# Optimization experiments

Measured on AMD Instinct MI355X. Metric: run time of the kernel, lower is better.

## Reference

```python
import jax, jax.numpy as jnp
import numpy as np

N = 3072      # nodes
F = 256       # nfeat
H = 8         # heads
H1 = 128      # hidden layer 1 (per head)
H2 = 128      # hidden layer 2 (per head)
OUT = 64      # out_att output dim
ALPHA = 0.2   # LeakyReLU slope
NEG = -9e15   # mask fill (as in dense GAT)


def setup_inputs() -> dict:
    key = jax.random.key(0)
    ks = jax.random.split(key, 11)
    x = jax.random.normal(ks[0], (N, F), jnp.float32)
    adj = jax.random.bernoulli(ks[1], 0.05, (N, N)).astype(jnp.float32)
    observation = jax.random.randint(ks[2], (1, N), 0, 2).astype(jnp.int32)
    s_mat = jax.random.bernoulli(ks[3], 0.05, (N, N)).astype(jnp.float32)  # unused (method='base')
    theta = jax.random.uniform(ks[4], (1, F), jnp.float32)
    W0 = jax.random.normal(ks[5], (H, F, H1), jnp.float32) * 0.05
    a0 = jax.random.normal(ks[6], (H, 2 * H1, 1), jnp.float32) * 0.05
    W1 = jax.random.normal(ks[7], (H, H1, H2), jnp.float32) * 0.05
    a1 = jax.random.normal(ks[8], (H, 2 * H2, 1), jnp.float32) * 0.05
    Wo = jax.random.normal(ks[9], (H * H2, OUT), jnp.float32) * 0.05
    ao = jax.random.normal(ks[10], (2 * OUT, 1), jnp.float32) * 0.05
    return {"x": x, "adj": adj, "observation": observation, "s_mat": s_mat,
            "theta": theta, "W0": W0, "a0": a0, "W1": W1, "a1": a1,
            "Wo": Wo, "ao": ao}


def _gat_layer(h, mask, W, a, concat):
    # Dense GAT layer: Wh = hW; e_ij = LeakyReLU(a1.Wh_i + a2.Wh_j); masked softmax; aggregate.
    Wh = h @ W                      # [N, d]
    d = W.shape[-1]
    f1 = Wh @ a[:d]                 # [N, 1]
    f2 = Wh @ a[d:]                 # [N, 1]
    e = jax.nn.leaky_relu(f1 + f2.T, ALPHA)           # [N, N]
    att = jax.nn.softmax(jnp.where(mask, e, NEG), axis=-1)
    hp = att @ Wh                   # [N, d]
    return jax.nn.elu(hp) if concat else hp


def reference(x, adj, observation, s_mat, theta, W0, a0, W1, a1, Wo, ao):
    mask = adj > 0
    # mergeState: add theta to rows of x in the seed set
    seed = (observation[0] == 1).astype(x.dtype)[:, None]   # [N, 1]
    h = x + seed * theta                                    # [N, F]
    # 8 heads, 2 stacked inner layers each (concat=True -> ELU inside)
    h0 = jax.vmap(lambda W, a: _gat_layer(h, mask, W, a, True))(W0, a0)          # [H, N, H1]
    h1 = jax.vmap(lambda hh, W, a: _gat_layer(hh, mask, W, a, True))(h0, W1, a1)  # [H, N, H2]
    hc = jnp.transpose(h1, (1, 0, 2)).reshape(N, H * H2)    # concat heads along features
    out = _gat_layer(hc, mask, Wo, ao, False)               # [N, OUT]
    return jax.nn.elu(out)
```

## Files before the change

### kernel.cpp

```cpp
#include <hip/hip_runtime.h>
#include <hip/hip_bf16.h>

#define NN 3072
#define NWORD 96
#define HH 8

typedef short short8 __attribute__((ext_vector_type(8)));
typedef float float4v __attribute__((ext_vector_type(4)));
typedef unsigned short ushort4v __attribute__((ext_vector_type(4)));

__device__ __forceinline__ float bf2f(unsigned short u) {
  union { unsigned u; float f; } v; v.u = ((unsigned)u) << 16; return v.f;
}
__device__ __forceinline__ unsigned short f2bf(float f) {
  union { float f; unsigned u; } v; v.f = f;
  unsigned r = v.u + 0x7fffu + ((v.u >> 16) & 1u);
  return (unsigned short)(r >> 16);
}
__device__ __forceinline__ float ldin(const void* p, size_t i, int isbf) {
  return isbf ? bf2f(((const unsigned short*)p)[i]) : ((const float*)p)[i];
}

__global__ __launch_bounds__(256) void k_detect(const unsigned* __restrict__ aw,
                                                int* __restrict__ flag) {
  __shared__ int s;
  if (threadIdx.x == 0) s = 0;
  __syncthreads();
  int any = 0;
  for (int i = threadIdx.x; i < 16384; i += 256)
    any |= ((aw[i] & 0xFFFFu) != 0u);
  if (any) s = 1;
  __syncthreads();
  if (threadIdx.x == 0) *flag = s;
}

__global__ __launch_bounds__(256) void k_mask(const void* __restrict__ adj,
                                              const int* __restrict__ flag,
                                              unsigned* __restrict__ maskT) {
  int isbf = *flag;
  int t = threadIdx.x;
  int lane = t & 63;
  for (int chunk = blockIdx.x; chunk < NN * 12; chunk += gridDim.x) {
    int row = chunk / 12;
    int seg = chunk - row * 12;
    int j = seg * 256 + t;
    bool pred = ldin(adj, (size_t)row * NN + j, isbf) != 0.f;
    unsigned long long b = __ballot(pred);
    int word = seg * 8 + (t >> 6) * 2;
    if (lane == 0) maskT[(size_t)word * NN + row] = (unsigned)b;
    else if (lane == 32) maskT[(size_t)(word + 1) * NN + row] = (unsigned)(b >> 32);
  }
}

__global__ __launch_bounds__(256) void k_prep(const void* __restrict__ x,
                                              const int* __restrict__ obs,
                                              const void* __restrict__ theta,
                                              const void* __restrict__ W0,
                                              const void* __restrict__ W1,
                                              const void* __restrict__ Wo,
                                              const int* __restrict__ flag,
                                              unsigned short* __restrict__ h_bf,
                                              unsigned short* __restrict__ W0T,
                                              unsigned short* __restrict__ W1T,
                                              unsigned short* __restrict__ WoT) {
  __shared__ __align__(16) unsigned short tile[16][17];
  int isbf = *flag;
  int t = threadIdx.x;
  int b = blockIdx.x;
  if (b < NN / 4) {
    for (int i = b * 1024 + t; i < b * 1024 + 1024; i += 256) {
      int row = i >> 8, c = i & 255;
      float v = ldin(x, i, isbf);
      if (obs[row] == 1) v += ldin(theta, c, isbf);
      h_bf[i] = f2bf(v);
    }
    return;
  }
  b -= NN / 4;
  const void* in; unsigned short* out; int R, C, r0, c0;
  if (b < 1024) {
    int h = b >> 7, rem = b & 127;
    in = (const char*)W0 + (size_t)h * 256 * 128 * (isbf ? 2 : 4);
    out = W0T + (size_t)h * 256 * 128;
    R = 256; C = 128; r0 = (rem >> 3) * 16; c0 = (rem & 7) * 16;
  } else if (b < 1536) {
    b -= 1024;
    int h = b >> 6, rem = b & 63;
    in = (const char*)W1 + (size_t)h * 128 * 128 * (isbf ? 2 : 4);
    out = W1T + (size_t)h * 128 * 128;
    R = 128; C = 128; r0 = (rem >> 3) * 16; c0 = (rem & 7) * 16;
  } else {
    b -= 1536;
    in = Wo; out = WoT;
    R = 1024; C = 64; r0 = (b >> 2) * 16; c0 = (b & 3) * 16;
  }
  int tc = t & 15, tr = t >> 4;
  tile[tr][tc] = f2bf(ldin(in, (size_t)(r0 + tr) * C + (c0 + tc), isbf));
  __syncthreads();
  out[(size_t)(c0 + tr) * R + (r0 + tc)] = tile[tc][tr];
}

template<int K>
__global__ __launch_bounds__(256) void k_gemm_fused(const unsigned short* __restrict__ A,
                                                    const unsigned short* __restrict__ WT,
                                                    unsigned short* __restrict__ WhTf,
                                                    long aOff, long wOff,
                                                    const void* __restrict__ avec,
                                                    const int* __restrict__ flag,
                                                    float* __restrict__ f1,
                                                    float* __restrict__ f2) {
  __shared__ __align__(16) unsigned short tile[4][2][32][17];
  __shared__ float avs[256];
  __shared__ float fp[2][8][32];
  int isbf = *flag;
  int head = blockIdx.x % HH;
  int jb = blockIdx.x / HH;
  A += (size_t)head * aOff; WT += (size_t)head * wOff;
  int rowbase = jb * 32;
  int t = threadIdx.x;
  int w = t >> 6, lane = t & 63;
  int q = lane >> 4, l = lane & 15;
  int colbase = w * 32;
  avs[t] = ldin(avec, (size_t)head * 256 + t, isbf);
  float4v acc[2][2];
#pragma unroll
  for (int rt = 0; rt < 2; rt++)
#pragma unroll
    for (int ct = 0; ct < 2; ct++) { float4v z = {0.f, 0.f, 0.f, 0.f}; acc[rt][ct] = z; }

  for (int kb = 0; kb < K; kb += 32) {
    short8 af[2], bfr[2];
#pragma unroll
    for (int rt = 0; rt < 2; rt++)
      af[rt] = *(const short8*)(A + (size_t)(rowbase + rt * 16 + l) * K + kb + q * 8);
#pragma unroll
    for (int ct = 0; ct < 2; ct++)
      bfr[ct] = *(const short8*)(WT + (size_t)(colbase + ct * 16 + l) * K + kb + q * 8);
#pragma unroll
    for (int rt = 0; rt < 2; rt++)
#pragma unroll
      for (int ct = 0; ct < 2; ct++)
        acc[rt][ct] = __builtin_amdgcn_mfma_f32_16x16x32_bf16(af[rt], bfr[ct], acc[rt][ct], 0, 0, 0);
  }
#pragma unroll
  for (int rt = 0; rt < 2; rt++)
#pragma unroll
    for (int ct = 0; ct < 2; ct++)
#pragma unroll
      for (int reg = 0; reg < 4; reg++)
        tile[w][ct][rt * 16 + q * 4 + reg][l] = f2bf(acc[rt][ct][reg]);
  __syncthreads();
#pragma unroll
  for (int ct = 0; ct < 2; ct++) {
    short8 r8;
#pragma unroll
    for (int i = 0; i < 8; i++) r8[i] = tile[w][ct][q * 8 + i][l];
    size_t chunk = ((size_t)head * (NN / 32) + jb) * 8 + (w * 2 + ct);
    *(short8*)(WhTf + chunk * 512 + lane * 8) = r8;
  }
  {
    int r = t & 31, g = t >> 5;
    int ww = g >> 1, cc = g & 1;
    float s1 = 0.f, s2 = 0.f;
#pragma unroll
    for (int li = 0; li < 16; li++) {
      float v = bf2f(tile[ww][cc][r][li]);
      s1 += v * avs[g * 16 + li];
      s2 += v * avs[128 + g * 16 + li];
    }
    fp[0][g][r] = s1; fp[1][g][r] = s2;
  }
  __syncthreads();
  if (t < 32) {
    float s1 = 0.f, s2 = 0.f;
#pragma unroll
    for (int g2 = 0; g2 < 8; g2++) { s1 += fp[0][g2][t]; s2 += fp[1][g2][t]; }
    f1[head * NN + rowbase + t] = s1;
    f2[head * NN + rowbase + t] = s2;
  }
}

template<int K, int KS>
__global__ __launch_bounds__(256) void k_gemm_out(const unsigned short* __restrict__ A,
                                                  const unsigned short* __restrict__ WT,
                                                  float* __restrict__ gpart) {
  constexpr int KC = K / KS;
  int ks = blockIdx.y;
  int rowbase = blockIdx.x * 16;
  int t = threadIdx.x;
  int w = t >> 6, lane = t & 63;
  int q = lane >> 4, l = lane & 15;
  int colbase = w * 16;
  float4v acc = {0.f, 0.f, 0.f, 0.f};
  for (int kb = ks * KC; kb < ks * KC + KC; kb += 32) {
    short8 af = *(const short8*)(A + (size_t)(rowbase + l) * K + kb + q * 8);
    short8 bfr = *(const short8*)(WT + (size_t)(colbase + l) * K + kb + q * 8);
    acc = __builtin_amdgcn_mfma_f32_16x16x32_bf16(af, bfr, acc, 0, 0, 0);
  }
#pragma unroll
  for (int reg = 0; reg < 4; reg++) {
    int r = rowbase + q * 4 + reg;
    int n = colbase + l;
    gpart[((size_t)ks * 64 + n) * NN + r] = acc[reg];
  }
}

template<int KS>
__global__ __launch_bounds__(256) void k_gemm_red(const float* __restrict__ gpart,
                                                  unsigned short* __restrict__ WhoTf) {
  int tid = blockIdx.x * 256 + threadIdx.x;
  int r = tid % NN, n = tid / NN;
  float s = 0.f;
#pragma unroll
  for (int ks = 0; ks < KS; ks++) s += gpart[((size_t)ks * 64 + n) * NN + r];
  int jb = r >> 5, q = (r >> 3) & 3, i = r & 7, ct = n >> 4, l = n & 15;
  WhoTf[((size_t)(jb * 4 + ct)) * 512 + (q * 16 + l) * 8 + i] = f2bf(s);
}

template<int DC>
__global__ __launch_bounds__(256) void k_f12f(const unsigned short* __restrict__ WhTf,
                                              const void* __restrict__ avec,
                                              const int* __restrict__ flag,
                                              float* __restrict__ f1, float* __restrict__ f2) {
  constexpr int NCT = DC / 16;
  int isbf = *flag;
  int head = blockIdx.y;
  int w = threadIdx.x >> 6, lane = threadIdx.x & 63;
  int q = lane >> 4, l = lane & 15;
  int jbIdx = blockIdx.x * 4 + w;
  size_t abase = (size_t)head * 2 * DC;
  float s1[8], s2[8];
#pragma unroll
  for (int i = 0; i < 8; i++) { s1[i] = 0.f; s2[i] = 0.f; }
#pragma unroll
  for (int ct = 0; ct < NCT; ct++) {
    short8 v = *(const short8*)(WhTf + (((size_t)head * (NN / 32) + jbIdx) * NCT + ct) * 512 + lane * 8);
    float a1v = ldin(avec, abase + ct * 16 + l, isbf);
    float a2v = ldin(avec, abase + DC + ct * 16 + l, isbf);
#pragma unroll
    for (int i = 0; i < 8; i++) {
      float f = bf2f((unsigned short)v[i]);
      s1[i] += f * a1v;
      s2[i] += f * a2v;
    }
  }
#pragma unroll
  for (int d = 1; d < 16; d <<= 1)
#pragma unroll
    for (int i = 0; i < 8; i++) {
      s1[i] += __shfl_xor(s1[i], d, 64);
      s2[i] += __shfl_xor(s2[i], d, 64);
    }
  if (l == 0) {
    int r = jbIdx * 32 + q * 8;
#pragma unroll
    for (int i = 0; i < 8; i++) {
      f1[head * NN + r + i] = s1[i];
      f2[head * NN + r + i] = s2[i];
    }
  }
}

template<int DCOL, int S>
__global__ __launch_bounds__(256, 4) void k_attn_part(
    const unsigned* __restrict__ maskT,
    const float* __restrict__ f1g, const float* __restrict__ f2g,
    const unsigned short* __restrict__ WhTf,
    unsigned short* __restrict__ pnum, float* __restrict__ pden, int NH) {
  constexpr int NCT = DCOL / 16;
  constexpr int JCH = NN / S;
  constexpr int NIT = JCH / 32;
  constexpr int CH = NCT * 512;
  constexpr int GR = CH / (256 * 8);
  __shared__ __align__(16) unsigned short Bs[2][CH];
  __shared__ __align__(16) float f2s[JCH];
  __shared__ unsigned ms[NIT * 64];

  int blk = blockIdx.x;
  int head = blk % NH;
  int rest = blk / NH;
  int js = rest % S;
  int bx = rest / S;
  int t = threadIdx.x;
  int w = t >> 6, lane = t & 63;
  int q = lane >> 4, l = lane & 15;
  int rowblk = bx * 64;
  int rowbase = rowblk + w * 16;
  size_t headJB = (size_t)head * (NN / 32);
  int j0 = js * JCH;

  for (int i = t; i < JCH; i += 256) f2s[i] = f2g[head * NN + j0 + i];
  for (int i = t; i < NIT * 64; i += 256)
    ms[i] = maskT[(size_t)((j0 >> 5) + (i >> 6)) * NN + rowblk + (i & 63)];
  float f1c = f1g[head * NN + rowbase + l] * 1.44269504f;

  short8 ones;
#pragma unroll
  for (int i = 0; i < 8; i++) ones[i] = (short)0x3F80;

  float4v acc[NCT];
#pragma unroll
  for (int ct = 0; ct < NCT; ct++) { float4v z = {0.f, 0.f, 0.f, 0.f}; acc[ct] = z; }
  float4v accd = {0.f, 0.f, 0.f, 0.f};

  short8 stg[GR];
  {
    const unsigned short* g0 = WhTf + (headJB + (j0 >> 5)) * (size_t)CH;
#pragma unroll
    for (int g = 0; g < GR; g++) stg[g] = *(const short8*)(g0 + g * 2048 + t * 8);
  }

  int cur = 0;
  for (int it = 0; it < NIT; it++) {
#pragma unroll
    for (int g = 0; g < GR; g++)
      *(short8*)(&Bs[cur][g * 2048 + t * 8]) = stg[g];
    __syncthreads();
    int itn = (it + 1 < NIT) ? it + 1 : 0;
    const unsigned short* gn = WhTf + (headJB + (j0 >> 5) + itn) * (size_t)CH;
#pragma unroll
    for (int g = 0; g < GR; g++) stg[g] = *(const short8*)(gn + g * 2048 + t * 8);

    unsigned mwc = ms[it * 64 + (w * 16 + l)] >> (q * 8);
    float4v fac = *(const float4v*)(&f2s[it * 32 + q * 8]);
    float4v fbc = *(const float4v*)(&f2s[it * 32 + q * 8 + 4]);
    short8 bfr[NCT];
#pragma unroll
    for (int ct = 0; ct < NCT; ct++)
      bfr[ct] = *(const short8*)(&Bs[cur][ct * 512 + lane * 8]);

    float p[8];
#pragma unroll
    for (int i = 0; i < 8; i++) {
      float fv = (i < 4) ? fac[i] : fbc[i - 4];
      float t0 = fmaf(fv, 1.44269504f, f1c);
      t0 = __builtin_amdgcn_fmed3f(t0, 0.2f * t0, 43.f);
      t0 = (mwc & (1u << i)) ? t0 : -200.f;
      p[i] = exp2f(t0);
    }
    union { __hip_bfloat162 b2[4]; short8 s8; } u0;
#pragma unroll
    for (int k = 0; k < 4; k++)
      u0.b2[k] = __float22bfloat162_rn({p[2 * k], p[2 * k + 1]});
    accd = __builtin_amdgcn_mfma_f32_16x16x32_bf16(u0.s8, ones, accd, 0, 0, 0);
#pragma unroll
    for (int ct = 0; ct < NCT; ct++)
      acc[ct] = __builtin_amdgcn_mfma_f32_16x16x32_bf16(u0.s8, bfr[ct], acc[ct], 0, 0, 0);
    cur ^= 1;
  }

  size_t slab = (size_t)(js * NH + head);
  if (l == 0) {
#pragma unroll
    for (int reg = 0; reg < 4; reg++)
      pden[slab * NN + rowbase + q * 4 + reg] = accd[reg];
  }
  int trb = rowbase >> 4;
#pragma unroll
  for (int ct = 0; ct < NCT; ct++) {
    ushort4v u;
    u.x = f2bf(acc[ct].x); u.y = f2bf(acc[ct].y);
    u.z = f2bf(acc[ct].z); u.w = f2bf(acc[ct].w);
    size_t cidx = ((slab * (NN / 16) + trb) * NCT + ct) * 256 + lane * 4;
    *(ushort4v*)(pnum + cidx) = u;
  }
}

template<int DCOL, int S>
__global__ __launch_bounds__(256) void k_attn_reduce(
    const unsigned short* __restrict__ pnum, const float* __restrict__ pden,
    void* __restrict__ outg, long outHeadOff, int outRowStride, int NH,
    const int* __restrict__ flag, int finalOut) {
  constexpr int NCT = DCOL / 16;
  int blk = blockIdx.x;
  int h = blk % NH;
  int bi = blk / NH;
  int t = threadIdx.x;
  int base = bi * 1024 + t * 4;
  int tile = base >> 8;
  int lane = (base >> 2) & 63;
  int ct = tile % NCT, tr = tile / NCT;
  int q = lane >> 4, l = lane & 15;
  int row0 = tr * 16 + q * 4;
  int col = ct * 16 + l;
  float sn[4] = {0.f, 0.f, 0.f, 0.f};
  float sd[4] = {0.f, 0.f, 0.f, 0.f};
#pragma unroll
  for (int js = 0; js < S; js++) {
    size_t sl = (size_t)(js * NH + h);
    ushort4v pv = *(const ushort4v*)(pnum + sl * (size_t)(NN * DCOL) + base);
    float4v dv = *(const float4v*)(pden + sl * NN + row0);
    sn[0] += bf2f(pv.x); sn[1] += bf2f(pv.y); sn[2] += bf2f(pv.z); sn[3] += bf2f(pv.w);
    sd[0] += dv.x; sd[1] += dv.y; sd[2] += dv.z; sd[3] += dv.w;
  }
  int f32o = finalOut && (*flag == 0);
#pragma unroll
  for (int r = 0; r < 4; r++) {
    float v = sd[r] > 0.f ? sn[r] / sd[r] : 0.f;
    v = v > 0.f ? v : expm1f(v);
    size_t idx = (size_t)h * outHeadOff + (size_t)(row0 + r) * outRowStride + col;
    if (f32o) ((float*)outg)[idx] = v;
    else ((unsigned short*)outg)[idx] = f2bf(v);
  }
}

extern "C" void kernel_launch(void* const* d_in, const int* in_sizes, int n_in,
                              void* d_out, int out_size, void* d_ws, size_t ws_size,
                              hipStream_t stream) {
  const void* x     = d_in[0];
  const void* adj   = d_in[1];
  const int*  obs   = (const int*)d_in[2];
  const void* theta = d_in[4];
  const void* W0    = d_in[5];
  const void* a0    = d_in[6];
  const void* W1    = d_in[7];
  const void* a1    = d_in[8];
  const void* Wo    = d_in[9];
  const void* ao    = d_in[10];

  char* ws = (char*)d_ws;
  size_t off = 0;
  auto alloc = [&](size_t bytes) { void* p = ws + off; off += (bytes + 255) & ~(size_t)255; return p; };
  int*            flag  = (int*)alloc(4);
  unsigned*       maskT = (unsigned*)alloc((size_t)NN * NWORD * 4);
  unsigned short* h_bf  = (unsigned short*)alloc((size_t)NN * 256 * 2);
  unsigned short* WhTf  = (unsigned short*)alloc((size_t)HH * 128 * NN * 2);
  float*          f1    = (float*)alloc((size_t)HH * NN * 4);
  float*          f2    = (float*)alloc((size_t)HH * NN * 4);
  unsigned short* h0    = (unsigned short*)alloc((size_t)HH * NN * 128 * 2);
  unsigned short* hc    = (unsigned short*)alloc((size_t)NN * 1024 * 2);
  unsigned short* W0T   = (unsigned short*)alloc((size_t)HH * 128 * 256 * 2);
  unsigned short* W1T   = (unsigned short*)alloc((size_t)HH * 128 * 128 * 2);
  unsigned short* WoT   = (unsigned short*)alloc((size_t)64 * 1024 * 2);
  unsigned short* WhoTf = (unsigned short*)alloc((size_t)64 * NN * 2);
  float*          fo1   = (float*)alloc((size_t)NN * 4);
  float*          fo2   = (float*)alloc((size_t)NN * 4);
  float*          gpart = (float*)alloc((size_t)4 * 64 * NN * 4);

  unsigned short* pnum = (unsigned short*)alloc((size_t)4 * HH * NN * 128 * 2);
  float* pden = (float*)alloc((size_t)32 * NN * 4);

  k_detect<<<1, 256, 0, stream>>>((const unsigned*)adj, flag);
  k_mask<<<1536, 256, 0, stream>>>(adj, flag, maskT);
  k_prep<<<NN / 4 + 1792, 256, 0, stream>>>(x, obs, theta, W0, W1, Wo, flag,
                                            h_bf, W0T, W1T, WoT);

  k_gemm_fused<256><<<(NN / 32) * HH, 256, 0, stream>>>(h_bf, W0T, WhTf,
                                                        0, 128 * 256, a0, flag, f1, f2);
  k_attn_part<128, 4><<<(NN / 64) * 4 * HH, 256, 0, stream>>>(maskT, f1, f2, WhTf, pnum, pden, HH);
  k_attn_reduce<128, 4><<<HH * NN * 128 / 1024, 256, 0, stream>>>(pnum, pden, h0, (long)NN * 128, 128, HH, flag, 0);
  k_gemm_fused<128><<<(NN / 32) * HH, 256, 0, stream>>>(h0, W1T, WhTf,
                                                        (long)NN * 128, 128 * 128, a1, flag, f1, f2);
  k_attn_part<128, 4><<<(NN / 64) * 4 * HH, 256, 0, stream>>>(maskT, f1, f2, WhTf, pnum, pden, HH);
  k_attn_reduce<128, 4><<<HH * NN * 128 / 1024, 256, 0, stream>>>(pnum, pden, hc, 128, 1024, HH, flag, 0);
  k_gemm_out<1024, 4><<<dim3(NN / 16, 4), 256, 0, stream>>>(hc, WoT, gpart);
  k_gemm_red<4><<<64 * NN / 256, 256, 0, stream>>>(gpart, WhoTf);
  k_f12f<64><<<dim3(NN / 128, 1), 256, 0, stream>>>(WhoTf, ao, flag, fo1, fo2);
  k_attn_part<64, 32><<<(NN / 64) * 32, 256, 0, stream>>>(maskT, fo1, fo2, WhoTf, pnum, pden, 1);
  k_attn_reduce<64, 32><<<NN * 64 / 1024, 256, 0, stream>>>(pnum, pden, d_out, 0, 64, 1, flag, 1);
}
```

Baseline: 305.4 us.

## Fuse attention reductions into following GEMMs and merge setup kernels

Folds the split-K attention reduction (normalise plus ELU) into the prologue of the next layer's GEMM, for both layer 1 and the output projection. This removes the h0 and hc intermediate buffers and two kernel launches. The dtype-detect, mask-build and prep kernels become one kernel, with each kernel re-detecting bf16 inline, and the gpart reduction is merged with the f1/f2 projection. Each GEMM block now recomputes its reduction from the partial sums, which adds global reads and divisions per block, and every kernel repeats a small detection read.

New measurement: 274.7 us. -10.0%, faster.

```diff
diff --git a/kernel.cpp b/kernel.cpp
--- a/kernel.cpp
+++ b/kernel.cpp
@@ -2,7 +2,6 @@
 #include <hip/hip_bf16.h>
 
 #define NN 3072
-#define NWORD 96
 #define HH 8
 
 typedef short short8 __attribute__((ext_vector_type(8)));
@@ -20,53 +19,45 @@
 __device__ __forceinline__ float ldin(const void* p, size_t i, int isbf) {
   return isbf ? bf2f(((const unsigned short*)p)[i]) : ((const float*)p)[i];
 }
-
-__global__ __launch_bounds__(256) void k_detect(const unsigned* __restrict__ aw,
-                                                int* __restrict__ flag) {
-  __shared__ int s;
-  if (threadIdx.x == 0) s = 0;
-  __syncthreads();
-  int any = 0;
-  for (int i = threadIdx.x; i < 16384; i += 256)
-    any |= ((aw[i] & 0xFFFFu) != 0u);
-  if (any) s = 1;
-  __syncthreads();
-  if (threadIdx.x == 0) *flag = s;
-}
-
-__global__ __launch_bounds__(256) void k_mask(const void* __restrict__ adj,
-                                              const int* __restrict__ flag,
-                                              unsigned* __restrict__ maskT) {
-  int isbf = *flag;
-  int t = threadIdx.x;
-  int lane = t & 63;
-  for (int chunk = blockIdx.x; chunk < NN * 12; chunk += gridDim.x) {
-    int row = chunk / 12;
-    int seg = chunk - row * 12;
-    int j = seg * 256 + t;
-    bool pred = ldin(adj, (size_t)row * NN + j, isbf) != 0.f;
-    unsigned long long b = __ballot(pred);
-    int word = seg * 8 + (t >> 6) * 2;
-    if (lane == 0) maskT[(size_t)word * NN + row] = (unsigned)b;
-    else if (lane == 32) maskT[(size_t)(word + 1) * NN + row] = (unsigned)(b >> 32);
-  }
-}
-
-__global__ __launch_bounds__(256) void k_prep(const void* __restrict__ x,
-                                              const int* __restrict__ obs,
-                                              const void* __restrict__ theta,
-                                              const void* __restrict__ W0,
-                                              const void* __restrict__ W1,
-                                              const void* __restrict__ Wo,
-                                              const int* __restrict__ flag,
-                                              unsigned short* __restrict__ h_bf,
-                                              unsigned short* __restrict__ W0T,
-                                              unsigned short* __restrict__ W1T,
-                                              unsigned short* __restrict__ WoT) {
+__device__ __forceinline__ int detect_bf(const void* adj) {
+  const unsigned* aw = (const unsigned*)adj;
+  int lane = threadIdx.x & 63;
+  unsigned o = 0;
+#pragma unroll
+  for (int i = 0; i < 16; i++) o |= aw[lane + i * 64] & 0xFFFFu;
+  return __ballot(o != 0) != 0ull;
+}
+
+__global__ __launch_bounds__(256) void k_maskprep(const void* __restrict__ adj,
+                                                  unsigned* __restrict__ maskT,
+                                                  const void* __restrict__ x,
+                                                  const int* __restrict__ obs,
+                                                  const void* __restrict__ theta,
+                                                  const void* __restrict__ W0,
+                                                  const void* __restrict__ W1,
+                                                  const void* __restrict__ Wo,
+                                                  unsigned short* __restrict__ h_bf,
+                                                  unsigned short* __restrict__ W0T,
+                                                  unsigned short* __restrict__ W1T,
+                                                  unsigned short* __restrict__ WoT) {
   __shared__ __align__(16) unsigned short tile[16][17];
-  int isbf = *flag;
-  int t = threadIdx.x;
-  int b = blockIdx.x;
+  int isbf = detect_bf(adj);
+  int t = threadIdx.x;
+  if (blockIdx.x < 1536) {
+    int lane = t & 63;
+    for (int chunk = blockIdx.x; chunk < NN * 12; chunk += 1536) {
+      int row = chunk / 12;
+      int seg = chunk - row * 12;
+      int j = seg * 256 + t;
+      bool pred = ldin(adj, (size_t)row * NN + j, isbf) != 0.f;
+      unsigned long long b = __ballot(pred);
+      int word = seg * 8 + (t >> 6) * 2;
+      if (lane == 0) maskT[(size_t)word * NN + row] = (unsigned)b;
+      else if (lane == 32) maskT[(size_t)(word + 1) * NN + row] = (unsigned)(b >> 32);
+    }
+    return;
+  }
+  int b = blockIdx.x - 1536;
   if (b < NN / 4) {
     for (int i = b * 1024 + t; i < b * 1024 + 1024; i += 256) {
       int row = i >> 8, c = i & 255;
@@ -106,13 +97,13 @@
                                                     unsigned short* __restrict__ WhTf,
                                                     long aOff, long wOff,
                                                     const void* __restrict__ avec,
-                                                    const int* __restrict__ flag,
+                                                    const void* __restrict__ adj,
                                                     float* __restrict__ f1,
                                                     float* __restrict__ f2) {
   __shared__ __align__(16) unsigned short tile[4][2][32][17];
   __shared__ float avs[256];
   __shared__ float fp[2][8][32];
-  int isbf = *flag;
+  int isbf = detect_bf(adj);
   int head = blockIdx.x % HH;
   int jb = blockIdx.x / HH;
   A += (size_t)head * aOff; WT += (size_t)head * wOff;
@@ -180,84 +171,202 @@
   }
 }
 
-template<int K, int KS>
-__global__ __launch_bounds__(256) void k_gemm_out(const unsigned short* __restrict__ A,
-                                                  const unsigned short* __restrict__ WT,
-                                                  float* __restrict__ gpart) {
-  constexpr int KC = K / KS;
-  int ks = blockIdx.y;
-  int rowbase = blockIdx.x * 16;
+__global__ __launch_bounds__(256) void k_gemm_fused2(
+    const unsigned short* __restrict__ pnumIn, const float* __restrict__ pdenIn,
+    const unsigned short* __restrict__ WT, unsigned short* __restrict__ WhTf,
+    long wOff, const void* __restrict__ avec, const void* __restrict__ adj,
+    float* __restrict__ f1, float* __restrict__ f2) {
+  constexpr int K = 128;
+  __shared__ __align__(16) unsigned short At[32][132];
+  __shared__ __align__(16) unsigned short tile[4][2][32][17];
+  __shared__ float avs[256];
+  __shared__ float fp[2][8][32];
+  int isbf = detect_bf(adj);
+  int head = blockIdx.x % HH;
+  int jb = blockIdx.x / HH;
+  WT += (size_t)head * wOff;
+  int rowbase = jb * 32;
   int t = threadIdx.x;
   int w = t >> 6, lane = t & 63;
   int q = lane >> 4, l = lane & 15;
+  int colbase = w * 32;
+  avs[t] = ldin(avec, (size_t)head * 256 + t, isbf);
+
+#pragma unroll
+  for (int c = 0; c < 4; c++) {
+    int e_loc = c * 1024 + t * 4;
+    int tloc = e_loc >> 8;
+    int trb_loc = tloc >> 3, ct = tloc & 7;
+    int lane_e = (e_loc >> 2) & 63;
+    int row0 = (2 * jb + trb_loc) * 16 + (lane_e >> 4) * 4;
+    int col = ct * 16 + (lane_e & 15);
+    float sn[4] = {0.f, 0.f, 0.f, 0.f};
+    float sd[4] = {0.f, 0.f, 0.f, 0.f};
+#pragma unroll
+    for (int js = 0; js < 4; js++) {
+      size_t sl = (size_t)(js * HH + head);
+      ushort4v pv = *(const ushort4v*)(pnumIn + sl * (size_t)(NN * 128) + jb * 4096 + e_loc);
+      float4v dv = *(const float4v*)(pdenIn + sl * NN + row0);
+      sn[0] += bf2f(pv.x); sn[1] += bf2f(pv.y); sn[2] += bf2f(pv.z); sn[3] += bf2f(pv.w);
+      sd[0] += dv.x; sd[1] += dv.y; sd[2] += dv.z; sd[3] += dv.w;
+    }
+    int lr0 = trb_loc * 16 + (lane_e >> 4) * 4;
+#pragma unroll
+    for (int r = 0; r < 4; r++) {
+      float v = sd[r] > 0.f ? sn[r] / sd[r] : 0.f;
+      v = v > 0.f ? v : expm1f(v);
+      At[lr0 + r][col] = f2bf(v);
+    }
+  }
+  __syncthreads();
+
+  float4v acc[2][2];
+#pragma unroll
+  for (int rt = 0; rt < 2; rt++)
+#pragma unroll
+    for (int ct = 0; ct < 2; ct++) { float4v z = {0.f, 0.f, 0.f, 0.f}; acc[rt][ct] = z; }
+
+  for (int kb = 0; kb < K; kb += 32) {
+    short8 af[2], bfr[2];
+#pragma unroll
+    for (int rt = 0; rt < 2; rt++)
+      af[rt] = *(const short8*)(&At[rt * 16 + l][kb + q * 8]);
+#pragma unroll
+    for (int ct = 0; ct < 2; ct++)
+      bfr[ct] = *(const short8*)(WT + (size_t)(colbase + ct * 16 + l) * K + kb + q * 8);
+#pragma unroll
+    for (int rt = 0; rt < 2; rt++)
+#pragma unroll
+      for (int ct = 0; ct < 2; ct++)
+        acc[rt][ct] = __builtin_amdgcn_mfma_f32_16x16x32_bf16(af[rt], bfr[ct], acc[rt][ct], 0, 0, 0);
+  }
+  __syncthreads();
+#pragma unroll
+  for (int rt = 0; rt < 2; rt++)
+#pragma unroll
+    for (int ct = 0; ct < 2; ct++)
+#pragma unroll
+      for (int reg = 0; reg < 4; reg++)
+        tile[w][ct][rt * 16 + q * 4 + reg][l] = f2bf(acc[rt][ct][reg]);
+  __syncthreads();
+#pragma unroll
+  for (int ct = 0; ct < 2; ct++) {
+    short8 r8;
+#pragma unroll
+    for (int i = 0; i < 8; i++) r8[i] = tile[w][ct][q * 8 + i][l];
+    size_t chunk = ((size_t)head * (NN / 32) + jb) * 8 + (w * 2 + ct);
+    *(short8*)(WhTf + chunk * 512 + lane * 8) = r8;
+  }
+  {
+    int r = t & 31, g = t >> 5;
+    int ww = g >> 1, cc = g & 1;
+    float s1 = 0.f, s2 = 0.f;
+#pragma unroll
+    for (int li = 0; li < 16; li++) {
+      float v = bf2f(tile[ww][cc][r][li]);
+      s1 += v * avs[g * 16 + li];
+      s2 += v * avs[128 + g * 16 + li];
+    }
+    fp[0][g][r] = s1; fp[1][g][r] = s2;
+  }
+  __syncthreads();
+  if (t < 32) {
+    float s1 = 0.f, s2 = 0.f;
+#pragma unroll
+    for (int g2 = 0; g2 < 8; g2++) { s1 += fp[0][g2][t]; s2 += fp[1][g2][t]; }
+    f1[head * NN + rowbase + t] = s1;
+    f2[head * NN + rowbase + t] = s2;
+  }
+}
+
+__global__ __launch_bounds__(256) void k_gemm_out_red(
+    const unsigned short* __restrict__ pnumIn, const float* __restrict__ pdenIn,
+    const unsigned short* __restrict__ WT, float* __restrict__ gpart) {
+  constexpr int K = 1024;
+  __shared__ __align__(16) unsigned short At[16][260];
+  int bx = blockIdx.x, ks = blockIdx.y;
+  int t = threadIdx.x;
+  int w = t >> 6, lane = t & 63;
+  int q = lane >> 4, l = lane & 15;
+#pragma unroll
+  for (int c = 0; c < 4; c++) {
+    int idx = c * 1024 + t * 4;
+    int hsel = idx >> 11;
+    int rem = idx & 2047;
+    int tloc = rem >> 8;
+    int lane_e = (rem >> 2) & 63;
+    int h = 2 * ks + hsel;
+    int row0 = bx * 16 + (lane_e >> 4) * 4;
+    int col = hsel * 128 + tloc * 16 + (lane_e & 15);
+    float sn[4] = {0.f, 0.f, 0.f, 0.f};
+    float sd[4] = {0.f, 0.f, 0.f, 0.f};
+#pragma unroll
+    for (int js = 0; js < 4; js++) {
+      size_t sl = (size_t)(js * HH + h);
+      ushort4v pv = *(const ushort4v*)(pnumIn + sl * (size_t)(NN * 128) + (bx * 8 + tloc) * 256 + (rem & 255));
+      float4v dv = *(const float4v*)(pdenIn + sl * NN + row0);
+      sn[0] += bf2f(pv.x); sn[1] += bf2f(pv.y); sn[2] += bf2f(pv.z); sn[3] += bf2f(pv.w);
+      sd[0] += dv.x; sd[1] += dv.y; sd[2] += dv.z; sd[3] += dv.w;
+    }
+    int lr0 = (lane_e >> 4) * 4;
+#pragma unroll
+    for (int r = 0; r < 4; r++) {
+      float v = sd[r] > 0.f ? sn[r] / sd[r] : 0.f;
+      v = v > 0.f ? v : expm1f(v);
+      At[lr0 + r][col] = f2bf(v);
+    }
+  }
+  __syncthreads();
+
   int colbase = w * 16;
   float4v acc = {0.f, 0.f, 0.f, 0.f};
-  for (int kb = ks * KC; kb < ks * KC + KC; kb += 32) {
-    short8 af = *(const short8*)(A + (size_t)(rowbase + l) * K + kb + q * 8);
-    short8 bfr = *(const short8*)(WT + (size_t)(colbase + l) * K + kb + q * 8);
+  for (int kb = 0; kb < 256; kb += 32) {
+    short8 af = *(const short8*)(&At[l][kb + q * 8]);
+    short8 bfr = *(const short8*)(WT + (size_t)(colbase + l) * K + ks * 256 + kb + q * 8);
     acc = __builtin_amdgcn_mfma_f32_16x16x32_bf16(af, bfr, acc, 0, 0, 0);
   }
 #pragma unroll
   for (int reg = 0; reg < 4; reg++) {
-    int r = rowbase + q * 4 + reg;
+    int r = bx * 16 + q * 4 + reg;
     int n = colbase + l;
     gpart[((size_t)ks * 64 + n) * NN + r] = acc[reg];
   }
 }
 
-template<int KS>
-__global__ __launch_bounds__(256) void k_gemm_red(const float* __restrict__ gpart,
-                                                  unsigned short* __restrict__ WhoTf) {
-  int tid = blockIdx.x * 256 + threadIdx.x;
-  int r = tid % NN, n = tid / NN;
-  float s = 0.f;
-#pragma unroll
-  for (int ks = 0; ks < KS; ks++) s += gpart[((size_t)ks * 64 + n) * NN + r];
-  int jb = r >> 5, q = (r >> 3) & 3, i = r & 7, ct = n >> 4, l = n & 15;
-  WhoTf[((size_t)(jb * 4 + ct)) * 512 + (q * 16 + l) * 8 + i] = f2bf(s);
-}
-
-template<int DC>
-__global__ __launch_bounds__(256) void k_f12f(const unsigned short* __restrict__ WhTf,
-                                              const void* __restrict__ avec,
-                                              const int* __restrict__ flag,
-                                              float* __restrict__ f1, float* __restrict__ f2) {
-  constexpr int NCT = DC / 16;
-  int isbf = *flag;
-  int head = blockIdx.y;
-  int w = threadIdx.x >> 6, lane = threadIdx.x & 63;
-  int q = lane >> 4, l = lane & 15;
-  int jbIdx = blockIdx.x * 4 + w;
-  size_t abase = (size_t)head * 2 * DC;
-  float s1[8], s2[8];
-#pragma unroll
-  for (int i = 0; i < 8; i++) { s1[i] = 0.f; s2[i] = 0.f; }
-#pragma unroll
-  for (int ct = 0; ct < NCT; ct++) {
-    short8 v = *(const short8*)(WhTf + (((size_t)head * (NN / 32) + jbIdx) * NCT + ct) * 512 + lane * 8);
-    float a1v = ldin(avec, abase + ct * 16 + l, isbf);
-    float a2v = ldin(avec, abase + DC + ct * 16 + l, isbf);
-#pragma unroll
-    for (int i = 0; i < 8; i++) {
-      float f = bf2f((unsigned short)v[i]);
-      s1[i] += f * a1v;
-      s2[i] += f * a2v;
-    }
-  }
-#pragma unroll
-  for (int d = 1; d < 16; d <<= 1)
-#pragma unroll
-    for (int i = 0; i < 8; i++) {
-      s1[i] += __shfl_xor(s1[i], d, 64);
-      s2[i] += __shfl_xor(s2[i], d, 64);
-    }
-  if (l == 0) {
-    int r = jbIdx * 32 + q * 8;
-#pragma unroll
-    for (int i = 0; i < 8; i++) {
-      f1[head * NN + r + i] = s1[i];
-      f2[head * NN + r + i] = s2[i];
-    }
+__global__ __launch_bounds__(256) void k_gemm_red_f12(
+    const float* __restrict__ gpart, unsigned short* __restrict__ WhoTf,
+    const void* __restrict__ avec, const void* __restrict__ adj,
+    float* __restrict__ f1, float* __restrict__ f2) {
+  __shared__ float as_[128];
+  __shared__ float fp[2][8][32];
+  int isbf = detect_bf(adj);
+  int jb = blockIdx.x;
+  int t = threadIdx.x;
+  if (t < 128) as_[t] = ldin(avec, t, isbf);
+  __syncthreads();
+  int r = t & 31, ng = t >> 5;
+  int r_glob = jb * 32 + r;
+  float s1 = 0.f, s2 = 0.f;
+#pragma unroll
+  for (int k = 0; k < 8; k++) {
+    int n = ng * 8 + k;
+    float s = 0.f;
+#pragma unroll
+    for (int ks = 0; ks < 4; ks++)
+      s += gpart[((size_t)ks * 64 + n) * NN + r_glob];
+    int qd = r >> 3, i = r & 7, ct = n >> 4, ld = n & 15;
+    WhoTf[((size_t)(jb * 4 + ct)) * 512 + (qd * 16 + ld) * 8 + i] = f2bf(s);
+    s1 += s * as_[n];
+    s2 += s * as_[64 + n];
+  }
+  fp[0][ng][r] = s1; fp[1][ng][r] = s2;
+  __syncthreads();
+  if (t < 32) {
+    float a = 0.f, b = 0.f;
+#pragma unroll
+    for (int g = 0; g < 8; g++) { a += fp[0][g][t]; b += fp[1][g][t]; }
+    f1[jb * 32 + t] = a;
+    f2[jb * 32 + t] = b;
   }
 }
 
@@ -369,12 +478,10 @@
 template<int DCOL, int S>
 __global__ __launch_bounds__(256) void k_attn_reduce(
     const unsigned short* __restrict__ pnum, const float* __restrict__ pden,
-    void* __restrict__ outg, long outHeadOff, int outRowStride, int NH,
-    const int* __restrict__ flag, int finalOut) {
+    void* __restrict__ outg, const void* __restrict__ adj) {
   constexpr int NCT = DCOL / 16;
-  int blk = blockIdx.x;
-  int h = blk % NH;
-  int bi = blk / NH;
+  int isbf = detect_bf(adj);
+  int bi = blockIdx.x;
   int t = threadIdx.x;
   int base = bi * 1024 + t * 4;
   int tile = base >> 8;
@@ -387,19 +494,18 @@
   float sd[4] = {0.f, 0.f, 0.f, 0.f};
 #pragma unroll
   for (int js = 0; js < S; js++) {
-    size_t sl = (size_t)(js * NH + h);
+    size_t sl = (size_t)js;
     ushort4v pv = *(const ushort4v*)(pnum + sl * (size_t)(NN * DCOL) + base);
     float4v dv = *(const float4v*)(pden + sl * NN + row0);
     sn[0] += bf2f(pv.x); sn[1] += bf2f(pv.y); sn[2] += bf2f(pv.z); sn[3] += bf2f(pv.w);
     sd[0] += dv.x; sd[1] += dv.y; sd[2] += dv.z; sd[3] += dv.w;
   }
-  int f32o = finalOut && (*flag == 0);
 #pragma unroll
   for (int r = 0; r < 4; r++) {
     float v = sd[r] > 0.f ? sn[r] / sd[r] : 0.f;
     v = v > 0.f ? v : expm1f(v);
-    size_t idx = (size_t)h * outHeadOff + (size_t)(row0 + r) * outRowStride + col;
-    if (f32o) ((float*)outg)[idx] = v;
+    size_t idx = (size_t)(row0 + r) * DCOL + col;
+    if (!isbf) ((float*)outg)[idx] = v;
     else ((unsigned short*)outg)[idx] = f2bf(v);
   }
 }
@@ -421,14 +527,11 @@
   char* ws = (char*)d_ws;
   size_t off = 0;
   auto alloc = [&](size_t bytes) { void* p = ws + off; off += (bytes + 255) & ~(size_t)255; return p; };
-  int*            flag  = (int*)alloc(4);
-  unsigned*       maskT = (unsigned*)alloc((size_t)NN * NWORD * 4);
+  unsigned*       maskT = (unsigned*)alloc((size_t)NN * 96 * 4);
   unsigned short* h_bf  = (unsigned short*)alloc((size_t)NN * 256 * 2);
   unsigned short* WhTf  = (unsigned short*)alloc((size_t)HH * 128 * NN * 2);
   float*          f1    = (float*)alloc((size_t)HH * NN * 4);
   float*          f2    = (float*)alloc((size_t)HH * NN * 4);
-  unsigned short* h0    = (unsigned short*)alloc((size_t)HH * NN * 128 * 2);
-  unsigned short* hc    = (unsigned short*)alloc((size_t)NN * 1024 * 2);
   unsigned short* W0T   = (unsigned short*)alloc((size_t)HH * 128 * 256 * 2);
   unsigned short* W1T   = (unsigned short*)alloc((size_t)HH * 128 * 128 * 2);
   unsigned short* WoT   = (unsigned short*)alloc((size_t)64 * 1024 * 2);
@@ -436,26 +539,19 @@
   float*          fo1   = (float*)alloc((size_t)NN * 4);
   float*          fo2   = (float*)alloc((size_t)NN * 4);
   float*          gpart = (float*)alloc((size_t)4 * 64 * NN * 4);
-
-  unsigned short* pnum = (unsigned short*)alloc((size_t)4 * HH * NN * 128 * 2);
-  float* pden = (float*)alloc((size_t)32 * NN * 4);
-
-  k_detect<<<1, 256, 0, stream>>>((const unsigned*)adj, flag);
-  k_mask<<<1536, 256, 0, stream>>>(adj, flag, maskT);
-  k_prep<<<NN / 4 + 1792, 256, 0, stream>>>(x, obs, theta, W0, W1, Wo, flag,
-                                            h_bf, W0T, W1T, WoT);
-
+  unsigned short* pnum  = (unsigned short*)alloc((size_t)4 * HH * NN * 128 * 2);
+  float*          pden  = (float*)alloc((size_t)32 * NN * 4);
+
+  k_maskprep<<<4096, 256, 0, stream>>>(adj, maskT, x, obs, theta, W0, W1, Wo,
+                                       h_bf, W0T, W1T, WoT);
   k_gemm_fused<256><<<(NN / 32) * HH, 256, 0, stream>>>(h_bf, W0T, WhTf,
-                                                        0, 128 * 256, a0, flag, f1, f2);
+                                                        0, 128 * 256, a0, adj, f1, f2);
   k_attn_part<128, 4><<<(NN / 64) * 4 * HH, 256, 0, stream>>>(maskT, f1, f2, WhTf, pnum, pden, HH);
-  k_attn_reduce<128, 4><<<HH * NN * 128 / 1024, 256, 0, stream>>>(pnum, pden, h0, (long)NN * 128, 128, HH, flag, 0);
-  k_gemm_fused<128><<<(NN / 32) * HH, 256, 0, stream>>>(h0, W1T, WhTf,
-                                                        (long)NN * 128, 128 * 128, a1, flag, f1, f2);
+  k_gemm_fused2<<<(NN / 32) * HH, 256, 0, stream>>>(pnum, pden, W1T, WhTf,
+                                                    128 * 128, a1, adj, f1, f2);
   k_attn_part<128, 4><<<(NN / 64) * 4 * HH, 256, 0, stream>>>(maskT, f1, f2, WhTf, pnum, pden, HH);
-  k_attn_reduce<128, 4><<<HH * NN * 128 / 1024, 256, 0, stream>>>(pnum, pden, hc, 128, 1024, HH, flag, 0);
-  k_gemm_out<1024, 4><<<dim3(NN / 16, 4), 256, 0, stream>>>(hc, WoT, gpart);
-  k_gemm_red<4><<<64 * NN / 256, 256, 0, stream>>>(gpart, WhoTf);
-  k_f12f<64><<<dim3(NN / 128, 1), 256, 0, stream>>>(WhoTf, ao, flag, fo1, fo2);
+  k_gemm_out_red<<<dim3(NN / 16, 4), 256, 0, stream>>>(pnum, pden, WoT, gpart);
+  k_gemm_red_f12<<<NN / 32, 256, 0, stream>>>(gpart, WhoTf, ao, adj, fo1, fo2);
   k_attn_part<64, 32><<<(NN / 64) * 32, 256, 0, stream>>>(maskT, fo1, fo2, WhoTf, pnum, pden, 1);
-  k_attn_reduce<64, 32><<<NN * 64 / 1024, 256, 0, stream>>>(pnum, pden, d_out, 0, 64, 1, flag, 1);
-}
+  k_attn_reduce<64, 32><<<NN * 64 / 1024, 256, 0, stream>>>(pnum, pden, d_out, adj);
+}
```
